# Kernel tuning notes

Measured on AMD Instinct MI355X. Metric: run time of the kernel, lower is better.

Reference implementation:

```python
import jax, jax.numpy as jnp
import numpy as np
from jax import lax

EPS = 1e-06
QP_ITERS = 500  # unrolled mirror-descent iterations for the simplex QP


def mlp_embed(x, W1, b1, W2, b2):
    # embedding_net: 2-layer MLP, [B, N, in_dim] -> [B, N, embed_dim]
    h = jax.nn.relu(jnp.einsum('bni,ih->bnh', x, W1) + b1)
    return jnp.einsum('bnh,hd->bnd', h, W2) + b2


def batch_svdd(emb, eps):
    # emb: [B, S, D].  SVDD dual QP per task:
    #   min_a  a^T K a - diag(K)^T a   s.t.  a >= 0, sum(a) = 1
    # (Q = 2K, p = -diag(K), G = -I, h = 0, A = 1^T, b = 1 in the torch QPFunction call)
    B, S, D = emb.shape
    K = jnp.einsum('bsd,btd->bst', emb, emb) + eps * jnp.eye(S, dtype=emb.dtype)
    kdiag = jnp.diagonal(K, axis1=-2, axis2=-1)  # [B, S]
    # Solve on the simplex with exponentiated-gradient (mirror descent with KL),
    # which converges to the unique QP optimum (K is PD after the eps jitter).
    # Per-task step size from the Gershgorin bound: eta <= 1 / (2 * ||K||_inf).
    eta = 1.0 / (2.0 * jnp.max(jnp.sum(jnp.abs(K), axis=-1), axis=-1, keepdims=True))  # [B,1]
    a0 = jnp.full((B, S), 1.0 / S, dtype=emb.dtype)

    def step(a, _):
        g = 2.0 * jnp.einsum('bst,bt->bs', K, a) - kdiag  # grad of a^T K a - kdiag^T a
        a = jax.nn.softmax(jnp.log(a + 1e-30) - eta * g, axis=-1)
        return a, None

    alphas, _ = lax.scan(step, a0, None, length=QP_ITERS)
    centers = jnp.einsum('bs,bsd->bd', alphas, emb)  # sum(alphas * inputs, dim=1)
    return centers


def setup_inputs() -> dict:
    key = jax.random.key(0)
    ks = jax.random.split(key, 4)
    tasks, shot, n_query, in_dim, hid, emb = 256, 32, 64, 1024, 2048, 512
    support_inputs = jax.random.normal(ks[0], (tasks, shot, in_dim), jnp.float32)
    query_inputs = jax.random.normal(ks[1], (tasks, n_query, in_dim), jnp.float32)
    W1 = jax.random.normal(ks[2], (in_dim, hid), jnp.float32) / np.sqrt(in_dim)
    b1 = jnp.zeros((hid,), jnp.float32)
    W2 = jax.random.normal(ks[3], (hid, emb), jnp.float32) / np.sqrt(hid)
    b2 = jnp.zeros((emb,), jnp.float32)
    return {'support_inputs': support_inputs, 'query_inputs': query_inputs,
            'W1': W1, 'b1': b1, 'W2': W2, 'b2': b2}


def reference(support_inputs, query_inputs, W1, b1, W2, b2):
    support_emb = mlp_embed(support_inputs, W1, b1, W2, b2)  # [B, S, D]
    centers = batch_svdd(support_emb, EPS)                   # [B, D]
    query_emb = mlp_embed(query_inputs, W1, b1, W2, b2)      # [B, Q, D]
    logits = -jnp.sum((centers[:, None, :] - query_emb) ** 2, axis=-1)  # [B, Q]
    return logits
```

## Files before the change

### kernel.cpp

```cpp
#include <hip/hip_runtime.h>
#include <hip/hip_bf16.h>

typedef __attribute__((ext_vector_type(8))) short bf16x8;
typedef __attribute__((ext_vector_type(4))) float f32x4;
typedef __attribute__((ext_vector_type(4))) unsigned short us4;

__device__ __forceinline__ unsigned short bf16_rne(float f) {
  unsigned u = __float_as_uint(f);
  unsigned r = u + 0x7fffu + ((u >> 16) & 1u);
  return (unsigned short)(r >> 16);
}

__device__ __forceinline__ void gload16(const void* g, void* l) {
  typedef const __attribute__((address_space(1))) unsigned int* gas;
  typedef __attribute__((address_space(3))) unsigned int* las;
  __builtin_amdgcn_global_load_lds((gas)g, (las)l, 16, 0, 0);
}

__device__ __forceinline__ float lane_f(float v, int l) {
  return __int_as_float(__builtin_amdgcn_readlane(__float_as_int(v), l));
}

#define BAR() asm volatile("s_barrier" ::: "memory")
#define VMCNT4() asm volatile("s_waitcnt vmcnt(4)" ::: "memory")

__global__ __launch_bounds__(256) void castx(const float* __restrict__ sup,
                                             const float* __restrict__ qry,
                                             unsigned short* __restrict__ X) {
  const int stride = gridDim.x * blockDim.x;
  for (int i = blockIdx.x * blockDim.x + threadIdx.x; i < 6291456; i += stride) {
    float4 v = (i < 2097152) ? ((const float4*)sup)[i] : ((const float4*)qry)[i - 2097152];
    us4 o = { bf16_rne(v.x), bf16_rne(v.y), bf16_rne(v.z), bf16_rne(v.w) };
    *(us4*)(X + (size_t)i * 4) = o;
  }
}

__global__ __launch_bounds__(256) void transcast(const float* __restrict__ src,
                                                 unsigned short* __restrict__ dst,
                                                 int R, int C) {
  __shared__ float t[32][33];
  const int tx = threadIdx.x & 31, ty = threadIdx.x >> 5;
  const int c0 = blockIdx.x * 32, r0 = blockIdx.y * 32;
#pragma unroll
  for (int j = 0; j < 4; j++)
    t[ty + j * 8][tx] = src[(size_t)(r0 + ty + j * 8) * C + c0 + tx];
  __syncthreads();
#pragma unroll
  for (int j = 0; j < 4; j++)
    dst[(size_t)(c0 + ty + j * 8) * R + r0 + tx] = bf16_rne(t[tx][ty + j * 8]);
}

#define MFMA_Q(AO, BO, MOFF, NOFF)                                                  \
  __builtin_amdgcn_s_setprio(1);                                                    \
  _Pragma("unroll") for (int i_ = 0; i_ < 4; ++i_)                                  \
  _Pragma("unroll") for (int j_ = 0; j_ < 2; ++j_)                                  \
  _Pragma("unroll") for (int ks_ = 0; ks_ < 2; ++ks_)                               \
    acc[(MOFF) + i_][(NOFF) + j_] = __builtin_amdgcn_mfma_f32_16x16x32_bf16(        \
        AO[i_][ks_], BO[j_][ks_], acc[(MOFF) + i_][(NOFF) + j_], 0, 0, 0);          \
  __builtin_amdgcn_s_setprio(0);

#define RDA(KS, ACH, MH, I) \
  (*(const bf16x8*)(lsc + ((ACH) * 32768 + (MH) * 8192 + (I) * 2048) + ((KS) ? vA_1 : vA_0)))
#define RDB(KS, BCH, JI) \
  (*(const bf16x8*)(lsc + ((BCH) * 32768 + (JI) * 2048) + ((KS) ? vB_1 : vB_0)))

#define STG(GLP, CHOFF, HALF)                                                     \
  gload16((GLP) + (size_t)((HALF) * 128) * ld,                                    \
          (char*)ls + ((CHOFF) + (HALF) * 16384) + wid * 1024);                   \
  gload16((GLP) + (size_t)((HALF) * 128 + 64) * ld,                               \
          (char*)ls + ((CHOFF) + (HALF) * 16384 + 8192) + wid * 1024);

#define GITER(ACH, BCH, ASO, BSO, T1, T2)                                         \
  {                                                                               \
    const char* Ap = AgL + (size_t)(T1) * 128;                                    \
    const char* Bp = BgL + (size_t)(T2) * 128;                                    \
    _Pragma("unroll") for (int i = 0; i < 4; ++i) {                               \
      afr[i][0] = RDA(0, ACH, 0, i); afr[i][1] = RDA(1, ACH, 0, i);               \
    }                                                                             \
    _Pragma("unroll") for (int j = 0; j < 2; ++j) {                               \
      bfr0[j][0] = RDB(0, BCH, j); bfr0[j][1] = RDB(1, BCH, j);                   \
    }                                                                             \
    STG(Ap, ASO, 0);                                                              \
    BAR();                                                                        \
    MFMA_Q(afr, bfr0, 0, 0);                                                      \
    BAR();                                                                        \
    _Pragma("unroll") for (int j = 0; j < 2; ++j) {                               \
      bfr1[j][0] = RDB(0, BCH, 2 + j); bfr1[j][1] = RDB(1, BCH, 2 + j);           \
    }                                                                             \
    STG(Ap, ASO, 1);                                                              \
    BAR();                                                                        \
    MFMA_Q(afr, bfr1, 0, 2);                                                      \
    BAR();                                                                        \
    _Pragma("unroll") for (int i = 0; i < 4; ++i) {                               \
      afr[i][0] = RDA(0, ACH, 1, i); afr[i][1] = RDA(1, ACH, 1, i);               \
    }                                                                             \
    STG(Bp, BSO, 0);                                                              \
    BAR();                                                                        \
    MFMA_Q(afr, bfr1, 4, 2);                                                      \
    BAR();                                                                        \
    STG(Bp, BSO, 1);                                                              \
    VMCNT4();                                                                     \
    BAR();                                                                        \
    MFMA_Q(afr, bfr0, 4, 0);                                                      \
    BAR();                                                                        \
  }

template <int ACT, int OUTBF>
__global__ __launch_bounds__(512) void gemm256(const unsigned short* __restrict__ A,
                                               const unsigned short* __restrict__ BT,
                                               const float* __restrict__ bias,
                                               void* __restrict__ Cout,
                                               int M, int N, int K) {
  __shared__ __attribute__((aligned(16))) short ls[4][16384];
  const int tid = threadIdx.x, lane = tid & 63, wid = tid >> 6;
  const int wm = wid >> 2, wn = wid & 3;
  const int l15 = lane & 15, lg = lane >> 4;

  int lin = blockIdx.y * gridDim.x + blockIdx.x;
  int nwg = gridDim.x * gridDim.y;
  int swz = (lin & 7) * (nwg >> 3) + (lin >> 3);
  int bx = swz % gridDim.x, by = swz / gridDim.x;
  const int m0 = by * 256, n0 = bx * 256;

  const size_t ld = (size_t)K * 2;
  const char* Ag = (const char*)A + (size_t)m0 * ld;
  const char* Bg = (const char*)BT + (size_t)n0 * ld;
  const int NT = K >> 6;
  const char* lsc = (const char*)ls;

  const int swz4 = (l15 & 7) << 4;
  const int bk0 = (l15 * 128 + lg * 16) ^ swz4;
  const int bk1 = (l15 * 128 + 64 + lg * 16) ^ swz4;
  const int vA_0 = bk0 + wm * 16384, vA_1 = bk1 + wm * 16384;
  const int vB_0 = bk0 + wn * 8192 + 65536, vB_1 = bk1 + wn * 8192 + 65536;

  const int srcrow = wid * 8 + (lane >> 3);
  const int kperm = ((lane & 7) ^ (lane >> 3)) << 4;
  const char* AgL = Ag + (size_t)srcrow * ld + kperm;
  const char* BgL = Bg + (size_t)srcrow * ld + kperm;

  f32x4 acc[8][4] = {};
  bf16x8 afr[4][2], bfr0[2][2], bfr1[2][2];

  STG(AgL, 0, 0); STG(AgL, 0, 1);
  STG(BgL, 65536, 0); STG(BgL, 65536, 1);
  STG(BgL + 128, 98304, 0); STG(BgL + 128, 98304, 1);
  VMCNT4();
  BAR();

  for (int u = 0; u < NT; u += 2) {
    int t2a = u + 2; if (t2a >= NT) t2a = 0;
    GITER(0, 0, 32768, 65536, u + 1, t2a);
    int t1b = u + 2; if (t1b >= NT) t1b = 0;
    int t2b = u + 3; if (t2b >= NT) t2b -= NT;
    GITER(1, 1, 0, 98304, t1b, t2b);
  }

  float bv[4];
#pragma unroll
  for (int nf = 0; nf < 4; ++nf) bv[nf] = bias[n0 + wn * 64 + nf * 16 + l15];
#pragma unroll
  for (int mf = 0; mf < 8; ++mf) {
    int rbase = m0 + wm * 128 + mf * 16 + lg * 4;
#pragma unroll
    for (int nf = 0; nf < 4; ++nf) {
      int col = n0 + wn * 64 + nf * 16 + l15;
#pragma unroll
      for (int j = 0; j < 4; ++j) {
        float v = acc[mf][nf][j] + bv[nf];
        if (ACT) v = v > 0.f ? v : 0.f;
        size_t idx = (size_t)(rbase + j) * N + col;
        if (OUTBF) ((unsigned short*)Cout)[idx] = bf16_rne(v);
        else       ((float*)Cout)[idx] = v;
      }
    }
  }
}

__global__ __launch_bounds__(256) void makeK(const float* __restrict__ E,
                                             float* __restrict__ Km,
                                             float* __restrict__ eta2v) {
  __shared__ float es[32][512];
  const int b = blockIdx.x, tid = threadIdx.x;
  const float4* Eb = (const float4*)(E + (size_t)b * 32 * 512);
  float4* es4 = (float4*)&es[0][0];
  for (int i = tid; i < 32 * 128; i += 256) es4[i] = Eb[i];
  __syncthreads();

  const int s = tid >> 3, tq = tid & 7;
  const float4* rs4 = (const float4*)&es[s][0];
  const float4* rt0 = (const float4*)&es[tq * 4 + 0][0];
  const float4* rt1 = (const float4*)&es[tq * 4 + 1][0];
  const float4* rt2 = (const float4*)&es[tq * 4 + 2][0];
  const float4* rt3 = (const float4*)&es[tq * 4 + 3][0];
  float4 a0 = {0, 0, 0, 0}, a1 = {0, 0, 0, 0}, a2 = {0, 0, 0, 0}, a3 = {0, 0, 0, 0};
  for (int dd = 0; dd < 128; ++dd) {
    float4 av = rs4[dd];
    float4 b0 = rt0[dd], b1 = rt1[dd], b2 = rt2[dd], b3 = rt3[dd];
    a0.x = fmaf(av.x, b0.x, a0.x); a0.y = fmaf(av.y, b0.y, a0.y);
    a0.z = fmaf(av.z, b0.z, a0.z); a0.w = fmaf(av.w, b0.w, a0.w);
    a1.x = fmaf(av.x, b1.x, a1.x); a1.y = fmaf(av.y, b1.y, a1.y);
    a1.z = fmaf(av.z, b1.z, a1.z); a1.w = fmaf(av.w, b1.w, a1.w);
    a2.x = fmaf(av.x, b2.x, a2.x); a2.y = fmaf(av.y, b2.y, a2.y);
    a2.z = fmaf(av.z, b2.z, a2.z); a2.w = fmaf(av.w, b2.w, a2.w);
    a3.x = fmaf(av.x, b3.x, a3.x); a3.y = fmaf(av.y, b3.y, a3.y);
    a3.z = fmaf(av.z, b3.z, a3.z); a3.w = fmaf(av.w, b3.w, a3.w);
  }
  float kv[4] = { (a0.x + a0.y) + (a0.z + a0.w), (a1.x + a1.y) + (a1.z + a1.w),
                  (a2.x + a2.y) + (a2.z + a2.w), (a3.x + a3.y) + (a3.z + a3.w) };
  float p = 0.f;
#pragma unroll
  for (int j = 0; j < 4; j++) {
    if (s == tq * 4 + j) kv[j] += 1e-6f;
    p += fabsf(kv[j]);
    Km[(size_t)b * 1024 + s * 32 + tq * 4 + j] = kv[j];
  }
  p += __shfl_xor(p, 1); p += __shfl_xor(p, 2); p += __shfl_xor(p, 4);
  __syncthreads();
  float* rs = &es[0][0];
  if (tq == 0) rs[s] = p;
  __syncthreads();
  if (tid < 32) {
    float m = rs[tid];
    m = fmaxf(m, __shfl_xor(m, 1));
    m = fmaxf(m, __shfl_xor(m, 2));
    m = fmaxf(m, __shfl_xor(m, 4));
    m = fmaxf(m, __shfl_xor(m, 8));
    m = fmaxf(m, __shfl_xor(m, 16));
    if (tid == 0) eta2v[b] = 1.4426950408889634f / (2.0f * m);
  }
}

__global__ __launch_bounds__(256) void qp_kernel(const float* __restrict__ Km,
                                                 const float* __restrict__ eta2v,
                                                 float* __restrict__ alp) {
  const int lane = threadIdx.x & 63, wid = threadIdx.x >> 6;
  const int b = blockIdx.x * 4 + wid;
  const int s = lane & 31;
  const float* Kb = Km + (size_t)b * 1024;
  float kr[32];
#pragma unroll
  for (int i = 0; i < 8; i++) {
    float4 v = ((const float4*)(Kb + s * 32))[i];
    kr[i * 4 + 0] = v.x; kr[i * 4 + 1] = v.y; kr[i * 4 + 2] = v.z; kr[i * 4 + 3] = v.w;
  }
  const float kd = Kb[s * 33];
  const float eta2 = eta2v[b];
  const float c2 = eta2 * kd;
  const float m2n = -2.0f * eta2;
  float w = 0.03125f;
  for (int it = 0; it < 500; ++it) {
    float c0 = 0.f, c1 = 0.f, ca = 0.f, c3 = 0.f;
#pragma unroll
    for (int t = 0; t < 32; t += 4) {
      c0 = fmaf(kr[t + 0], lane_f(w, t + 0), c0);
      c1 = fmaf(kr[t + 1], lane_f(w, t + 1), c1);
      ca = fmaf(kr[t + 2], lane_f(w, t + 2), ca);
      c3 = fmaf(kr[t + 3], lane_f(w, t + 3), c3);
    }
    float tK = (c0 + c1) + (ca + c3);
    float r = w;
    r += __int_as_float(__builtin_amdgcn_update_dpp(0, __float_as_int(r), 0x128, 0xf, 0xf, true));
    r += __int_as_float(__builtin_amdgcn_update_dpp(0, __float_as_int(r), 0x124, 0xf, 0xf, true));
    r += __int_as_float(__builtin_amdgcn_update_dpp(0, __float_as_int(r), 0x122, 0xf, 0xf, true));
    r += __int_as_float(__builtin_amdgcn_update_dpp(0, __float_as_int(r), 0x121, 0xf, 0xf, true));
    r += __shfl_xor(r, 16);
    float R = __builtin_amdgcn_rcpf(r);
    float z = fmaf(m2n * R, tK, c2);
    w = w * R * __builtin_amdgcn_exp2f(z);
  }
  float r = w;
  r += __int_as_float(__builtin_amdgcn_update_dpp(0, __float_as_int(r), 0x128, 0xf, 0xf, true));
  r += __int_as_float(__builtin_amdgcn_update_dpp(0, __float_as_int(r), 0x124, 0xf, 0xf, true));
  r += __int_as_float(__builtin_amdgcn_update_dpp(0, __float_as_int(r), 0x122, 0xf, 0xf, true));
  r += __int_as_float(__builtin_amdgcn_update_dpp(0, __float_as_int(r), 0x121, 0xf, 0xf, true));
  r += __shfl_xor(r, 16);
  float R = __builtin_amdgcn_rcpf(r);
  if (lane < 32) alp[(size_t)b * 32 + s] = w * R;
}

__global__ __launch_bounds__(128) void centers_k(const float* __restrict__ alp,
                                                 const float* __restrict__ E,
                                                 float* __restrict__ ctr) {
  const int b = blockIdx.x, t = threadIdx.x;
  __shared__ float av[32];
  if (t < 32) av[t] = alp[(size_t)b * 32 + t];
  __syncthreads();
  const float4* Eb = (const float4*)(E + (size_t)b * 32 * 512);
  float4 c = {0, 0, 0, 0};
#pragma unroll 8
  for (int sIdx = 0; sIdx < 32; sIdx++) {
    float a = av[sIdx];
    float4 v = Eb[sIdx * 128 + t];
    c.x = fmaf(a, v.x, c.x); c.y = fmaf(a, v.y, c.y);
    c.z = fmaf(a, v.z, c.z); c.w = fmaf(a, v.w, c.w);
  }
  ((float4*)ctr)[b * 128 + t] = c;
}

__global__ __launch_bounds__(256) void logits_k(const float* __restrict__ ctr,
                                                const float* __restrict__ E,
                                                float* __restrict__ out) {
  const int b = blockIdx.x, lane = threadIdx.x & 63, w = threadIdx.x >> 6;
  const float4* C4 = (const float4*)(ctr + (size_t)b * 512);
  const float4 cA = C4[lane * 2], cB = C4[lane * 2 + 1];
  const float4* Q4 = (const float4*)(E + (size_t)(8192 + b * 64) * 512);
  for (int q = w; q < 64; q += 4) {
    float4 e0 = Q4[(size_t)q * 128 + lane * 2];
    float4 e1 = Q4[(size_t)q * 128 + lane * 2 + 1];
    float d, ss = 0.f;
    d = cA.x - e0.x; ss = fmaf(d, d, ss);
    d = cA.y - e0.y; ss = fmaf(d, d, ss);
    d = cA.z - e0.z; ss = fmaf(d, d, ss);
    d = cA.w - e0.w; ss = fmaf(d, d, ss);
    d = cB.x - e1.x; ss = fmaf(d, d, ss);
    d = cB.y - e1.y; ss = fmaf(d, d, ss);
    d = cB.z - e1.z; ss = fmaf(d, d, ss);
    d = cB.w - e1.w; ss = fmaf(d, d, ss);
    ss += __shfl_xor(ss, 1);  ss += __shfl_xor(ss, 2);  ss += __shfl_xor(ss, 4);
    ss += __shfl_xor(ss, 8);  ss += __shfl_xor(ss, 16); ss += __shfl_xor(ss, 32);
    if (lane == 0) out[b * 64 + q] = -ss;
  }
}

extern "C" void kernel_launch(void* const* d_in, const int* in_sizes, int n_in,
                              void* d_out, int out_size, void* d_ws, size_t ws_size,
                              hipStream_t stream) {
  const float* sup = (const float*)d_in[0];
  const float* qry = (const float*)d_in[1];
  const float* W1  = (const float*)d_in[2];
  const float* b1  = (const float*)d_in[3];
  const float* W2  = (const float*)d_in[4];
  const float* b2  = (const float*)d_in[5];
  float* out = (float*)d_out;

  char* ws = (char*)d_ws;
  unsigned short* H   = (unsigned short*)(ws);
  unsigned short* Xbf = (unsigned short*)(ws + 100663296);
  float* E    = (float*)(ws + 100663296);
  unsigned short* W1T = (unsigned short*)(ws + 150994944);
  unsigned short* W2T = (unsigned short*)(ws + 155189248);
  float* Km   = (float*)(ws + 157286400);
  float* eta2 = (float*)(ws + 158334976);
  float* alp  = (float*)(ws + 158336000);
  float* ctr  = (float*)(ws + 158368768);

  castx<<<dim3(2048), dim3(256), 0, stream>>>(sup, qry, Xbf);
  transcast<<<dim3(64, 32), dim3(256), 0, stream>>>(W1, W1T, 1024, 2048);
  transcast<<<dim3(16, 64), dim3(256), 0, stream>>>(W2, W2T, 2048, 512);
  gemm256<1, 1><<<dim3(8, 96), dim3(512), 0, stream>>>(Xbf, W1T, b1, (void*)H, 24576, 2048, 1024);
  gemm256<0, 0><<<dim3(2, 96), dim3(512), 0, stream>>>(H, W2T, b2, (void*)E, 24576, 512, 2048);
  makeK<<<dim3(256), dim3(256), 0, stream>>>(E, Km, eta2);
  qp_kernel<<<dim3(64), dim3(256), 0, stream>>>(Km, eta2, alp);
  centers_k<<<dim3(256), dim3(128), 0, stream>>>(alp, E, ctr);
  logits_k<<<dim3(256), dim3(256), 0, stream>>>(ctr, E, out);
}
```

Before: 308.6 us.

## Restructure GEMM main loop into double-buffered tiles with one barrier each

After: 303.5 us. About the same (-1.7%).

```diff
diff --git a/kernel.cpp b/kernel.cpp
--- a/kernel.cpp
+++ b/kernel.cpp
@@ -22,7 +22,10 @@
 }
 
 #define BAR() asm volatile("s_barrier" ::: "memory")
-#define VMCNT4() asm volatile("s_waitcnt vmcnt(4)" ::: "memory")
+#define VMCNT0() asm volatile("s_waitcnt vmcnt(0)" ::: "memory")
+#define LGKM4() asm volatile("s_waitcnt lgkmcnt(4)" ::: "memory")
+#define LGKM0() asm volatile("s_waitcnt lgkmcnt(0)" ::: "memory")
+#define SB() __builtin_amdgcn_sched_barrier(0)
 
 __global__ __launch_bounds__(256) void castx(const float* __restrict__ sup,
                                              const float* __restrict__ qry,
@@ -70,39 +73,33 @@
   gload16((GLP) + (size_t)((HALF) * 128 + 64) * ld,                               \
           (char*)ls + ((CHOFF) + (HALF) * 16384 + 8192) + wid * 1024);
 
-#define GITER(ACH, BCH, ASO, BSO, T1, T2)                                         \
+#define TILE(ACH, BCH, ASO, BSO, T)                                               \
   {                                                                               \
-    const char* Ap = AgL + (size_t)(T1) * 128;                                    \
-    const char* Bp = BgL + (size_t)(T2) * 128;                                    \
+    VMCNT0();                                                                     \
+    BAR();                                                                        \
     _Pragma("unroll") for (int i = 0; i < 4; ++i) {                               \
       afr[i][0] = RDA(0, ACH, 0, i); afr[i][1] = RDA(1, ACH, 0, i);               \
     }                                                                             \
     _Pragma("unroll") for (int j = 0; j < 2; ++j) {                               \
       bfr0[j][0] = RDB(0, BCH, j); bfr0[j][1] = RDB(1, BCH, j);                   \
     }                                                                             \
-    STG(Ap, ASO, 0);                                                              \
-    BAR();                                                                        \
-    MFMA_Q(afr, bfr0, 0, 0);                                                      \
-    BAR();                                                                        \
     _Pragma("unroll") for (int j = 0; j < 2; ++j) {                               \
       bfr1[j][0] = RDB(0, BCH, 2 + j); bfr1[j][1] = RDB(1, BCH, 2 + j);           \
     }                                                                             \
-    STG(Ap, ASO, 1);                                                              \
-    BAR();                                                                        \
+    const char* Ap_ = AgL + (size_t)(T) * 128;                                    \
+    const char* Bp_ = BgL + (size_t)(T) * 128;                                    \
+    STG(Ap_, ASO, 0); STG(Ap_, ASO, 1);                                           \
+    STG(Bp_, BSO, 0); STG(Bp_, BSO, 1);                                           \
+    LGKM4(); SB();                                                                \
+    MFMA_Q(afr, bfr0, 0, 0);                                                      \
+    LGKM0(); SB();                                                                \
     MFMA_Q(afr, bfr1, 0, 2);                                                      \
-    BAR();                                                                        \
     _Pragma("unroll") for (int i = 0; i < 4; ++i) {                               \
       afr[i][0] = RDA(0, ACH, 1, i); afr[i][1] = RDA(1, ACH, 1, i);               \
     }                                                                             \
-    STG(Bp, BSO, 0);                                                              \
-    BAR();                                                                        \
+    LGKM0(); SB();                                                                \
     MFMA_Q(afr, bfr1, 4, 2);                                                      \
-    BAR();                                                                        \
-    STG(Bp, BSO, 1);                                                              \
-    VMCNT4();                                                                     \
-    BAR();                                                                        \
     MFMA_Q(afr, bfr0, 4, 0);                                                      \
-    BAR();                                                                        \
   }
 
 template <int ACT, int OUTBF>
@@ -144,16 +141,12 @@
 
   STG(AgL, 0, 0); STG(AgL, 0, 1);
   STG(BgL, 65536, 0); STG(BgL, 65536, 1);
-  STG(BgL + 128, 98304, 0); STG(BgL + 128, 98304, 1);
-  VMCNT4();
-  BAR();
 
   for (int u = 0; u < NT; u += 2) {
-    int t2a = u + 2; if (t2a >= NT) t2a = 0;
-    GITER(0, 0, 32768, 65536, u + 1, t2a);
-    int t1b = u + 2; if (t1b >= NT) t1b = 0;
-    int t2b = u + 3; if (t2b >= NT) t2b -= NT;
-    GITER(1, 1, 0, 98304, t1b, t2b);
+    int t1 = u + 1;
+    int t2 = u + 2; if (t2 >= NT) t2 = 0;
+    TILE(0, 0, 32768, 98304, t1);
+    TILE(1, 1, 0, 65536, t2);
   }
 
   float bv[4];
```
